# Optimization experiments

Hardware: AMD Instinct MI355X
Metric: run time of the kernel (lower is better)

Reference implementation:

```python
import jax, jax.numpy as jnp
import numpy as np

B, N, D = 8, 256, 128
LN_EPS = 1e-5


def setup_inputs() -> dict:
    key = jax.random.key(0)
    ks = jax.random.split(key, 12)
    s = 0.02
    return {
        "node_features": jax.random.normal(ks[0], (B, N, D), dtype=jnp.float32),
        "adjacency": jax.random.uniform(ks[1], (B, N, N), dtype=jnp.float32),
        "msg_w1": jax.random.normal(ks[2], (2 * D, D), dtype=jnp.float32) * s,
        "msg_b1": jnp.zeros((D,), jnp.float32),
        "msg_w2": jax.random.normal(ks[3], (D, D), dtype=jnp.float32) * s,
        "msg_b2": jnp.zeros((D,), jnp.float32),
        "upd_w1": jax.random.normal(ks[4], (2 * D, D), dtype=jnp.float32) * s,
        "upd_b1": jnp.zeros((D,), jnp.float32),
        "upd_w2": jax.random.normal(ks[5], (D, D), dtype=jnp.float32) * s,
        "upd_b2": jnp.zeros((D,), jnp.float32),
        "ln_g": jnp.ones((D,), jnp.float32),
        "ln_b": jnp.zeros((D,), jnp.float32),
    }


def reference(node_features, adjacency, msg_w1, msg_b1, msg_w2, msg_b2,
              upd_w1, upd_b1, upd_w2, upd_b2, ln_g, ln_b):
    d = node_features.shape[-1]
    n = node_features.shape[1]
    # Split the concat-then-matmul: cat(x_i, x_j) @ W1 == x_i @ W1[:d] + x_j @ W1[d:]
    hi = node_features @ msg_w1[:d]          # [B,N,D] (receiver i contribution)
    hj = node_features @ msg_w1[d:]          # [B,N,D] (sender j contribution)
    h = jax.nn.relu(hi[:, :, None, :] + hj[:, None, :, :] + msg_b1)  # [B,N,N,D]
    # Edge weights with the i==j pairs excluded (loop skips self-edges)
    a = adjacency * (1.0 - jnp.eye(n, dtype=adjacency.dtype))        # [B,N,N]
    # sum_j (h @ W2 + b2) * a_ij  ==  (sum_j h * a_ij) @ W2 + b2 * sum_j a_ij
    s = jnp.einsum('bijd,bij->bid', h, a)    # [B,N,D]
    agg = s @ msg_w2 + msg_b2 * jnp.sum(a, axis=-1, keepdims=True)   # [B,N,D]
    u = jnp.concatenate([node_features, agg], axis=-1)               # [B,N,2D]
    upd = jax.nn.relu(u @ upd_w1 + upd_b1) @ upd_w2 + upd_b2         # [B,N,D]
    res = node_features + upd
    mu = jnp.mean(res, axis=-1, keepdims=True)
    var = jnp.var(res, axis=-1, keepdims=True)
    return (res - mu) / jnp.sqrt(var + LN_EPS) * ln_g + ln_b
```

## Files before the change

### kernel.cpp

```cpp
#include <hip/hip_runtime.h>

#define BB 8
#define NN 256
#define DD 128
#define LN_EPS 1e-5f

__global__ __launch_bounds__(1024, 4) void k_proj(const float* __restrict__ x,
                                                  const float* __restrict__ w1,
                                                  const float* __restrict__ b1,
                                                  float* __restrict__ hi,
                                                  float* __restrict__ hjb) {
    __shared__ float xs[8 * DD];
    __shared__ float part[16384];
    const int bid  = blockIdx.x;
    const int row0 = (bid & 7) * NN + (bid >> 3) * 8;
    const int tid  = threadIdx.x;
    xs[tid] = x[row0 * DD + tid];
    __syncthreads();

    const int dp = tid & 127;
    const int kg = tid >> 7;
    const int kb = kg * 16;

    float aA[8] = {}, aB[8] = {};
    #pragma unroll
    for (int k4 = 0; k4 < 4; ++k4) {
        const int k0 = kb + k4 * 4;
        float wa[4], wb[4];
        #pragma unroll
        for (int q = 0; q < 4; ++q) {
            wa[q] = w1[(k0 + q) * DD + dp];
            wb[q] = w1[(DD + k0 + q) * DD + dp];
        }
        #pragma unroll
        for (int r = 0; r < 8; ++r) {
            const float4 xv = *(const float4*)&xs[r * DD + k0];
            aA[r] = fmaf(xv.x, wa[0], aA[r]);
            aA[r] = fmaf(xv.y, wa[1], aA[r]);
            aA[r] = fmaf(xv.z, wa[2], aA[r]);
            aA[r] = fmaf(xv.w, wa[3], aA[r]);
            aB[r] = fmaf(xv.x, wb[0], aB[r]);
            aB[r] = fmaf(xv.y, wb[1], aB[r]);
            aB[r] = fmaf(xv.z, wb[2], aB[r]);
            aB[r] = fmaf(xv.w, wb[3], aB[r]);
        }
    }
    #pragma unroll
    for (int r = 0; r < 8; ++r) {
        part[kg * 1024 + r * DD + dp]        = aA[r];
        part[8192 + kg * 1024 + r * DD + dp] = aB[r];
    }
    __syncthreads();
    {
        int r = tid >> 7, d = tid & 127;
        float sa = 0.f, sb = 0.f;
        #pragma unroll
        for (int w = 0; w < 8; ++w) {
            sa += part[w * 1024 + r * DD + d];
            sb += part[8192 + w * 1024 + r * DD + d];
        }
        hi [(row0 + r) * DD + d] = sa;
        hjb[(row0 + r) * DD + d] = sb + b1[d];
    }
}

__global__ __launch_bounds__(1024, 4) void k_fused(const float* __restrict__ adj,
                                                   const float* __restrict__ x,
                                                   const float* __restrict__ hi,
                                                   const float* __restrict__ hjb,
                                                   const float* __restrict__ w2,
                                                   const float* __restrict__ b2,
                                                   const float* __restrict__ w3,
                                                   const float* __restrict__ b3,
                                                   const float* __restrict__ w4,
                                                   const float* __restrict__ b4,
                                                   const float* __restrict__ g,
                                                   const float* __restrict__ bet,
                                                   float* __restrict__ out) {
    __shared__ float smem[13320];
    float* const hjs    = smem;
    float* const partP  = smem;
    float* const partT  = smem;
    float* const a_t    = smem + 8192;
    float* const u1s    = smem + 8192;
    float* const resS   = smem + 9216;
    float* const xs     = smem + 10240;
    float* const ssp    = smem + 11264;
    float* const aggs   = smem + 12288;
    float* const asum_s = smem + 13312;

    const int bid = blockIdx.x;
    const int b   = bid & 7;
    const int i0  = (bid >> 3) * 8;
    const int tid = threadIdx.x;

    #pragma unroll
    for (int t = 0; t < 2; ++t) {
        int idx = tid + t * 1024;
        int il = idx >> 8, j = idx & 255;
        int ig = i0 + il;
        float av = adj[((size_t)b * NN + ig) * NN + j];
        a_t[il * 256 + j] = (j == ig) ? 0.f : av;
    }
    xs[tid] = x[((size_t)b * NN + i0) * DD + tid];
    __syncthreads();

    if (tid < 512) {
        int r = tid >> 6, l = tid & 63;
        float s = a_t[r * 256 + l] + a_t[r * 256 + l + 64]
                + a_t[r * 256 + l + 128] + a_t[r * 256 + l + 192];
        #pragma unroll
        for (int m = 32; m; m >>= 1) s += __shfl_xor(s, m);
        if (l == 0) asum_s[r] = s;
    }

    const int dq  = tid & 31;
    const int row = (tid >> 5) & 7;
    const int jh  = tid >> 8;
    const float4 hi4 = *(const float4*)&hi[((size_t)b * NN + i0 + row) * DD + dq * 4];
    float4 acc = {0.f, 0.f, 0.f, 0.f};

    for (int jt = 0; jt < 4; ++jt) {
        __syncthreads();
        const float4* src = (const float4*)(hjb + ((size_t)b * NN + jt * 64) * DD);
        float4* dst = (float4*)hjs;
        #pragma unroll
        for (int t = 0; t < 2; ++t) dst[tid + t * 1024] = src[tid + t * 1024];
        __syncthreads();
        const int jb = jh * 16;
        #pragma unroll 8
        for (int jj = 0; jj < 16; ++jj) {
            const int jl = jb + jj;
            const float4 hv = *(const float4*)&hjs[jl * 128 + dq * 4];
            const float a = a_t[row * 256 + jt * 64 + jl];
            acc.x = fmaf(fmaxf(hi4.x + hv.x, 0.f), a, acc.x);
            acc.y = fmaf(fmaxf(hi4.y + hv.y, 0.f), a, acc.y);
            acc.z = fmaf(fmaxf(hi4.z + hv.z, 0.f), a, acc.z);
            acc.w = fmaf(fmaxf(hi4.w + hv.w, 0.f), a, acc.w);
        }
    }
    __syncthreads();
    *(float4*)&partP[jh * 1024 + row * 128 + dq * 4] = acc;
    __syncthreads();
    {
        float s = partP[tid] + partP[1024 + tid] + partP[2048 + tid] + partP[3072 + tid];
        ssp[tid] = s;
    }
    __syncthreads();

    const int dp = tid & 127;
    const int kg = tid >> 7;
    const int kb = kg * 16;

    {
        float w0[16];
        #pragma unroll
        for (int k = 0; k < 16; ++k) w0[k] = w2[(kb + k) * DD + dp];
        #pragma unroll
        for (int r = 0; r < 8; ++r) {
            float a0 = 0.f;
            #pragma unroll
            for (int q = 0; q < 4; ++q) {
                const float4 sv = *(const float4*)&ssp[r * 128 + kb + q * 4];
                a0 = fmaf(sv.x, w0[q*4+0], a0);
                a0 = fmaf(sv.y, w0[q*4+1], a0);
                a0 = fmaf(sv.z, w0[q*4+2], a0);
                a0 = fmaf(sv.w, w0[q*4+3], a0);
            }
            partT[kg * 1024 + r * 128 + dp] = a0;
        }
    }
    __syncthreads();
    {
        int r = tid >> 7, d = tid & 127;
        float s = 0.f;
        #pragma unroll
        for (int w = 0; w < 8; ++w) s += partT[w * 1024 + tid];
        aggs[tid] = s + b2[d] * asum_s[r];
    }
    __syncthreads();

    {
        float wa0[16], wb0[16];
        #pragma unroll
        for (int k = 0; k < 16; ++k) {
            wa0[k] = w3[(kb + k) * DD + dp];
            wb0[k] = w3[(DD + kb + k) * DD + dp];
        }
        #pragma unroll
        for (int r = 0; r < 8; ++r) {
            float a0 = 0.f;
            #pragma unroll
            for (int q = 0; q < 4; ++q) {
                const float4 xv = *(const float4*)&xs[r * 128 + kb + q * 4];
                const float4 av = *(const float4*)&aggs[r * 128 + kb + q * 4];
                a0 = fmaf(xv.x, wa0[q*4+0], a0);
                a0 = fmaf(xv.y, wa0[q*4+1], a0);
                a0 = fmaf(xv.z, wa0[q*4+2], a0);
                a0 = fmaf(xv.w, wa0[q*4+3], a0);
                a0 = fmaf(av.x, wb0[q*4+0], a0);
                a0 = fmaf(av.y, wb0[q*4+1], a0);
                a0 = fmaf(av.z, wb0[q*4+2], a0);
                a0 = fmaf(av.w, wb0[q*4+3], a0);
            }
            partT[kg * 1024 + r * 128 + dp] = a0;
        }
    }
    __syncthreads();
    {
        int d = tid & 127;
        float s = 0.f;
        #pragma unroll
        for (int w = 0; w < 8; ++w) s += partT[w * 1024 + tid];
        u1s[tid] = fmaxf(s + b3[d], 0.f);
    }
    __syncthreads();

    {
        float w0[16];
        #pragma unroll
        for (int k = 0; k < 16; ++k) w0[k] = w4[(kb + k) * DD + dp];
        #pragma unroll
        for (int r = 0; r < 8; ++r) {
            float a0 = 0.f;
            #pragma unroll
            for (int q = 0; q < 4; ++q) {
                const float4 uv = *(const float4*)&u1s[r * 128 + kb + q * 4];
                a0 = fmaf(uv.x, w0[q*4+0], a0);
                a0 = fmaf(uv.y, w0[q*4+1], a0);
                a0 = fmaf(uv.z, w0[q*4+2], a0);
                a0 = fmaf(uv.w, w0[q*4+3], a0);
            }
            partT[kg * 1024 + r * 128 + dp] = a0;
        }
    }
    __syncthreads();
    {
        int d = tid & 127;
        float s = xs[tid] + b4[d];
        #pragma unroll
        for (int w = 0; w < 8; ++w) s += partT[w * 1024 + tid];
        resS[tid] = s;
    }
    __syncthreads();

    if (tid < 512) {
        const int r = tid >> 6, l = tid & 63;
        const float2 v = *(const float2*)&resS[r * 128 + l * 2];
        float s1 = v.x + v.y;
        float s2 = v.x * v.x + v.y * v.y;
        #pragma unroll
        for (int m = 32; m; m >>= 1) {
            s1 += __shfl_xor(s1, m);
            s2 += __shfl_xor(s2, m);
        }
        const float mu = s1 * (1.f / DD);
        const float rs = rsqrtf(s2 * (1.f / DD) - mu * mu + LN_EPS);
        const int d = l * 2;
        const float2 gv = *(const float2*)&g[d];
        const float2 bv = *(const float2*)&bet[d];
        float2 o;
        o.x = (v.x - mu) * rs * gv.x + bv.x;
        o.y = (v.y - mu) * rs * gv.y + bv.y;
        *(float2*)&out[((size_t)b * NN + i0 + r) * DD + d] = o;
    }
}

extern "C" void kernel_launch(void* const* d_in, const int* in_sizes, int n_in,
                              void* d_out, int out_size, void* d_ws, size_t ws_size,
                              hipStream_t stream) {
    (void)in_sizes; (void)n_in; (void)out_size; (void)ws_size;
    const float* x      = (const float*)d_in[0];
    const float* adj    = (const float*)d_in[1];
    const float* msg_w1 = (const float*)d_in[2];
    const float* msg_b1 = (const float*)d_in[3];
    const float* msg_w2 = (const float*)d_in[4];
    const float* msg_b2 = (const float*)d_in[5];
    const float* upd_w1 = (const float*)d_in[6];
    const float* upd_b1 = (const float*)d_in[7];
    const float* upd_w2 = (const float*)d_in[8];
    const float* upd_b2 = (const float*)d_in[9];
    const float* ln_g   = (const float*)d_in[10];
    const float* ln_b   = (const float*)d_in[11];
    float* out = (float*)d_out;

    const size_t BND = (size_t)BB * NN * DD;
    float* ws  = (float*)d_ws;
    float* hi  = ws;
    float* hjb = ws + BND;

    k_proj<<<dim3(256), dim3(1024), 0, stream>>>(x, msg_w1, msg_b1, hi, hjb);
    k_fused<<<dim3(256), dim3(1024), 0, stream>>>(adj, x, hi, hjb,
                                                  msg_w2, msg_b2,
                                                  upd_w1, upd_b1, upd_w2, upd_b2,
                                                  ln_g, ln_b, out);
}
```

Measured before the change: 24.96 us.

## Register-block four receiver rows per thread in edge aggregation loop

Each thread in the fused kernel now accumulates four receiver rows instead of one. Each sender-row load of hj from shared memory is therefore reused four times, and the per-thread j range shrinks to four per tile across sixteen waves. Adjacency is stored transposed so the four edge weights come from one float4 load. Row sums are computed with wave shuffles during the adjacency load, removing a separate pass. The cost is more registers per thread and a larger partial-sum reduction, now sixteen wave partials reduced in two staged passes with extra barriers.

```diff
diff --git a/kernel.cpp b/kernel.cpp
--- a/kernel.cpp
+++ b/kernel.cpp
@@ -77,22 +77,25 @@
                                                    const float* __restrict__ g,
                                                    const float* __restrict__ bet,
                                                    float* __restrict__ out) {
-    __shared__ float smem[13320];
+    __shared__ float smem[13352];
     float* const hjs    = smem;
     float* const partP  = smem;
     float* const partT  = smem;
-    float* const a_t    = smem + 8192;
+    float* const a_tt   = smem + 8192;
     float* const u1s    = smem + 8192;
     float* const resS   = smem + 9216;
     float* const xs     = smem + 10240;
     float* const ssp    = smem + 11264;
     float* const aggs   = smem + 12288;
-    float* const asum_s = smem + 13312;
-
-    const int bid = blockIdx.x;
-    const int b   = bid & 7;
-    const int i0  = (bid >> 3) * 8;
-    const int tid = threadIdx.x;
+    float* const asub   = smem + 13312;
+    float* const asum_s = smem + 13344;
+
+    const int bid  = blockIdx.x;
+    const int b    = bid & 7;
+    const int i0   = (bid >> 3) * 8;
+    const int tid  = threadIdx.x;
+    const int lane = tid & 63;
+    const int wv   = tid >> 6;
 
     #pragma unroll
     for (int t = 0; t < 2; ++t) {
@@ -100,25 +103,22 @@
         int il = idx >> 8, j = idx & 255;
         int ig = i0 + il;
         float av = adj[((size_t)b * NN + ig) * NN + j];
-        a_t[il * 256 + j] = (j == ig) ? 0.f : av;
+        av = (j == ig) ? 0.f : av;
+        a_tt[j * 8 + il] = av;
+        float s = av;
+        #pragma unroll
+        for (int m = 32; m; m >>= 1) s += __shfl_xor(s, m);
+        if (lane == 0) asub[il * 4 + ((idx >> 6) & 3)] = s;
     }
     xs[tid] = x[((size_t)b * NN + i0) * DD + tid];
-    __syncthreads();
-
-    if (tid < 512) {
-        int r = tid >> 6, l = tid & 63;
-        float s = a_t[r * 256 + l] + a_t[r * 256 + l + 64]
-                + a_t[r * 256 + l + 128] + a_t[r * 256 + l + 192];
-        #pragma unroll
-        for (int m = 32; m; m >>= 1) s += __shfl_xor(s, m);
-        if (l == 0) asum_s[r] = s;
-    }
-
-    const int dq  = tid & 31;
-    const int row = (tid >> 5) & 7;
-    const int jh  = tid >> 8;
-    const float4 hi4 = *(const float4*)&hi[((size_t)b * NN + i0 + row) * DD + dq * 4];
-    float4 acc = {0.f, 0.f, 0.f, 0.f};
+
+    const int dq = lane & 31;
+    const int rh = lane >> 5;
+    float4 hi4[4];
+    #pragma unroll
+    for (int rr = 0; rr < 4; ++rr)
+        hi4[rr] = *(const float4*)&hi[((size_t)b * NN + i0 + rh * 4 + rr) * DD + dq * 4];
+    float4 acc[4] = {{0,0,0,0},{0,0,0,0},{0,0,0,0},{0,0,0,0}};
 
     for (int jt = 0; jt < 4; ++jt) {
         __syncthreads();
@@ -127,23 +127,52 @@
         #pragma unroll
         for (int t = 0; t < 2; ++t) dst[tid + t * 1024] = src[tid + t * 1024];
         __syncthreads();
-        const int jb = jh * 16;
-        #pragma unroll 8
-        for (int jj = 0; jj < 16; ++jj) {
+        const int jb = wv * 4;
+        #pragma unroll
+        for (int jj = 0; jj < 4; ++jj) {
             const int jl = jb + jj;
-            const float4 hv = *(const float4*)&hjs[jl * 128 + dq * 4];
-            const float a = a_t[row * 256 + jt * 64 + jl];
-            acc.x = fmaf(fmaxf(hi4.x + hv.x, 0.f), a, acc.x);
-            acc.y = fmaf(fmaxf(hi4.y + hv.y, 0.f), a, acc.y);
-            acc.z = fmaf(fmaxf(hi4.z + hv.z, 0.f), a, acc.z);
-            acc.w = fmaf(fmaxf(hi4.w + hv.w, 0.f), a, acc.w);
-        }
-    }
-    __syncthreads();
-    *(float4*)&partP[jh * 1024 + row * 128 + dq * 4] = acc;
-    __syncthreads();
-    {
-        float s = partP[tid] + partP[1024 + tid] + partP[2048 + tid] + partP[3072 + tid];
+            const float4 hv = *(const float4*)&hjs[jl * DD + dq * 4];
+            const float4 a4 = *(const float4*)&a_tt[(jt * 64 + jl) * 8 + rh * 4];
+            const float aa[4] = {a4.x, a4.y, a4.z, a4.w};
+            #pragma unroll
+            for (int rr = 0; rr < 4; ++rr) {
+                acc[rr].x = fmaf(fmaxf(hi4[rr].x + hv.x, 0.f), aa[rr], acc[rr].x);
+                acc[rr].y = fmaf(fmaxf(hi4[rr].y + hv.y, 0.f), aa[rr], acc[rr].y);
+                acc[rr].z = fmaf(fmaxf(hi4[rr].z + hv.z, 0.f), aa[rr], acc[rr].z);
+                acc[rr].w = fmaf(fmaxf(hi4[rr].w + hv.w, 0.f), aa[rr], acc[rr].w);
+            }
+        }
+    }
+    __syncthreads();
+
+    if (wv < 8) {
+        float* pp = partP + wv * 1024 + rh * 4 * DD;
+        #pragma unroll
+        for (int rr = 0; rr < 4; ++rr)
+            *(float4*)&pp[rr * DD + dq * 4] = acc[rr];
+    }
+    __syncthreads();
+    if (tid < 8)
+        asum_s[tid] = asub[tid * 4] + asub[tid * 4 + 1]
+                    + asub[tid * 4 + 2] + asub[tid * 4 + 3];
+    {
+        float s = 0.f;
+        #pragma unroll
+        for (int w = 0; w < 8; ++w) s += partP[w * 1024 + tid];
+        ssp[tid] = s;
+    }
+    __syncthreads();
+    if (wv >= 8) {
+        float* pp = partP + (wv - 8) * 1024 + rh * 4 * DD;
+        #pragma unroll
+        for (int rr = 0; rr < 4; ++rr)
+            *(float4*)&pp[rr * DD + dq * 4] = acc[rr];
+    }
+    __syncthreads();
+    {
+        float s = ssp[tid];
+        #pragma unroll
+        for (int w = 0; w < 8; ++w) s += partP[w * 1024 + tid];
         ssp[tid] = s;
     }
     __syncthreads();
```

Result: slower. 26.85 us (+7.6%).
